# Kernel optimization log

Hardware: AMD Instinct MI355X
Metric: run time of the kernel (lower is better)

Reference implementation:

```python
import jax, jax.numpy as jnp
import numpy as np

T, B, D, H = 1024, 64, 1024, 30  # seq_len, batch, input_size, hidden_size


def setup_inputs() -> dict:
    key = jax.random.key(0)
    ks = jax.random.split(key, 11)
    sc = 1.0 / np.sqrt(H)  # torch default init scale ~ U(-1/sqrt(H), 1/sqrt(H))
    u = lambda k, shape: jax.random.uniform(k, shape, dtype=jnp.float32, minval=-sc, maxval=sc)
    return {
        "x": jax.random.normal(ks[0], (T, B, D), dtype=jnp.float32),
        "W_ih0": u(ks[1], (4 * H, D)),
        "W_hh0": u(ks[2], (4 * H, H)),
        "b_ih0": u(ks[3], (4 * H,)),
        "b_hh0": u(ks[4], (4 * H,)),
        "W_ih1": u(ks[5], (4 * H, H)),
        "W_hh1": u(ks[6], (4 * H, H)),
        "b_ih1": u(ks[7], (4 * H,)),
        "b_hh1": u(ks[8], (4 * H,)),
        "W_out": u(ks[9], (1, H)),
        "b_out": u(ks[10], (1,)),
    }


def _lstm_layer(xs, Wih, Whh, bih, bhh):
    # xs: [T, B, Din] -> hs: [T, B, H]. PyTorch gate order: i, f, g, o.
    xg = jnp.einsum("tbd,gd->tbg", xs, Wih) + (bih + bhh)  # precompute input projection
    h0 = jnp.zeros((xs.shape[1], H), xs.dtype)
    c0 = jnp.zeros((xs.shape[1], H), xs.dtype)

    def step(carry, xw):
        h, c = carry
        gates = xw + h @ Whh.T  # [B, 4H]
        i, f, g, o = jnp.split(gates, 4, axis=-1)
        c = jax.nn.sigmoid(f) * c + jax.nn.sigmoid(i) * jnp.tanh(g)
        h = jax.nn.sigmoid(o) * jnp.tanh(c)
        return (h, c), h

    _, hs = jax.lax.scan(step, (h0, c0), xg)
    return hs


def reference(x, W_ih0, W_hh0, b_ih0, b_hh0, W_ih1, W_hh1, b_ih1, b_hh1, W_out, b_out):
    h1 = _lstm_layer(x, W_ih0, W_hh0, b_ih0, b_hh0)   # layer 0
    h2 = _lstm_layer(h1, W_ih1, W_hh1, b_ih1, b_hh1)  # layer 1
    return h2 @ W_out.T + b_out  # [T, B, 1]
```

## Files before the change

### kernel.cpp

```cpp
#include <hip/hip_runtime.h>
#include <hip/hip_bf16.h>
#include <cstdint>

#define TT 1024
#define BB 64
#define DD 1024
#define HH 30
#define G4 120

typedef __attribute__((ext_vector_type(8))) short short8;
typedef __attribute__((ext_vector_type(4))) float float4v;

__device__ __forceinline__ float frcp(float x) { return __builtin_amdgcn_rcpf(x); }
__device__ __forceinline__ float fsig(float x) { return frcp(1.0f + __expf(-x)); }
__device__ __forceinline__ float ftan(float x) {
    return 2.0f * frcp(1.0f + __expf(-2.0f * x)) - 1.0f;
}
__device__ __forceinline__ float bcast(float v, int l) {
    return __int_as_float(__builtin_amdgcn_readlane(__float_as_int(v), l));
}
__device__ __forceinline__ unsigned short bf16_rne(float f) {
    unsigned u = __float_as_uint(f);
    return (unsigned short)((u + 0x7FFFu + ((u >> 16) & 1u)) >> 16);
}

__global__ void prep_kernel(const float* __restrict__ Wih0,
                            const float* __restrict__ bih0,
                            const float* __restrict__ bhh0,
                            unsigned short* __restrict__ Bhi,
                            unsigned short* __restrict__ Blo,
                            float* __restrict__ bias0) {
    int idx = blockIdx.x * 256 + threadIdx.x;
    int l  = idx & 63;
    int kc = (idx >> 6) & 31;
    int nt = idx >> 11;
    int n = nt * 16 + (l & 15);
    int kb = kc * 32 + (l >> 4) * 8;
    size_t o = (size_t)idx * 8;
#pragma unroll
    for (int j = 0; j < 8; ++j) {
        float wv = (n < G4) ? Wih0[(size_t)n * DD + kb + j] : 0.0f;
        unsigned short hi = bf16_rne(wv);
        float fhi = __uint_as_float((unsigned)hi << 16);
        unsigned short lo = bf16_rne(wv - fhi);
        Bhi[o + j] = hi;
        Blo[o + j] = lo;
    }
    if (idx < 128) bias0[idx] = (idx < G4) ? (bih0[idx] + bhh0[idx]) : 0.0f;
}

__global__ __launch_bounds__(256) void gemm_xg(
    const float* __restrict__ x, const unsigned short* __restrict__ Bhi,
    const unsigned short* __restrict__ Blo, const float* __restrict__ bias0,
    float* __restrict__ xgp) {
    const int tid = threadIdx.x;
    const int w = tid >> 6;
    const int l = tid & 63;
    const int lm = l & 15, lq = l >> 4;
    const int r0 = blockIdx.x * 128 + w * 32;

    float4v acc[2][8];
#pragma unroll
    for (int mt = 0; mt < 2; ++mt)
#pragma unroll
        for (int nt = 0; nt < 8; ++nt) acc[mt][nt] = (float4v)0.0f;

    const float* aptr[2];
    aptr[0] = x + (size_t)(r0 + lm) * DD + lq * 8;
    aptr[1] = x + (size_t)(r0 + 16 + lm) * DD + lq * 8;

    float4 pa[2][2];
#pragma unroll
    for (int mt = 0; mt < 2; ++mt) {
        pa[mt][0] = *(const float4*)(aptr[mt]);
        pa[mt][1] = *(const float4*)(aptr[mt] + 4);
    }

    for (int kc = 0; kc < 32; ++kc) {
        short8 ahi[2], alo[2];
#pragma unroll
        for (int mt = 0; mt < 2; ++mt) {
            float f[8] = {pa[mt][0].x, pa[mt][0].y, pa[mt][0].z, pa[mt][0].w,
                          pa[mt][1].x, pa[mt][1].y, pa[mt][1].z, pa[mt][1].w};
#pragma unroll
            for (int i = 0; i < 8; ++i) {
                unsigned ub = __float_as_uint(f[i]);
                ahi[mt][i] = (short)(ub >> 16);
                float fr = f[i] - __uint_as_float(ub & 0xFFFF0000u);
                alo[mt][i] = (short)(__float_as_uint(fr) >> 16);
            }
        }
        if (kc + 1 < 32) {
            const int ko = (kc + 1) * 32;
#pragma unroll
            for (int mt = 0; mt < 2; ++mt) {
                pa[mt][0] = *(const float4*)(aptr[mt] + ko);
                pa[mt][1] = *(const float4*)(aptr[mt] + ko + 4);
            }
        }
#pragma unroll
        for (int nt = 0; nt < 8; ++nt) {
            const size_t bo = ((size_t)(nt * 32 + kc) * 64 + l) * 8;
            short8 bh = *(const short8*)(Bhi + bo);
            short8 bl = *(const short8*)(Blo + bo);
            acc[0][nt] = __builtin_amdgcn_mfma_f32_16x16x32_bf16(ahi[0], bh, acc[0][nt], 0, 0, 0);
            acc[1][nt] = __builtin_amdgcn_mfma_f32_16x16x32_bf16(ahi[1], bh, acc[1][nt], 0, 0, 0);
            acc[0][nt] = __builtin_amdgcn_mfma_f32_16x16x32_bf16(alo[0], bh, acc[0][nt], 0, 0, 0);
            acc[1][nt] = __builtin_amdgcn_mfma_f32_16x16x32_bf16(alo[1], bh, acc[1][nt], 0, 0, 0);
            acc[0][nt] = __builtin_amdgcn_mfma_f32_16x16x32_bf16(ahi[0], bl, acc[0][nt], 0, 0, 0);
            acc[1][nt] = __builtin_amdgcn_mfma_f32_16x16x32_bf16(ahi[1], bl, acc[1][nt], 0, 0, 0);
        }
    }

#pragma unroll
    for (int nt = 0; nt < 8; ++nt) {
        const int g = nt * 16 + lm;
        if (g < G4) {
            const int gm = g % 60;
            const int lane_t = (gm < HH) ? gm : (32 + gm - HH);
            const int slot = g / 60;
            const float bb = bias0[g];
#pragma unroll
            for (int mt = 0; mt < 2; ++mt)
#pragma unroll
                for (int i = 0; i < 4; ++i) {
                    const size_t row = r0 + mt * 16 + lq * 4 + i;
                    xgp[(row * 64 + lane_t) * 2 + slot] = acc[mt][nt][i] + bb;
                }
        }
    }
}

__global__ __launch_bounds__(128, 1) void lstm_rec(
    const float* __restrict__ xgp, const float* __restrict__ Whh0,
    const float* __restrict__ Wih1, const float* __restrict__ Whh1,
    const float* __restrict__ bih1, const float* __restrict__ bhh1,
    float* __restrict__ h2buf) {
    const int tid = threadIdx.x;
    const int wv = tid >> 6;
    const int l = tid & 63;
    const int b = blockIdx.x;
    const int u = l & 31;
    const int half = l >> 5;
    const bool al = (u < HH);
    const int rlo = half * HH + (al ? u : 0);
    const int rhi = 60 + rlo;

    __shared__ float2 pg[2][64];

    float wa[HH], wb[HH], wc[HH], wd[HH];
    float b1lo = 0.f, b1hi = 0.f;
    if (wv == 0) {
#pragma unroll
        for (int j = 0; j < HH; ++j) {
            wa[j] = al ? Whh0[rlo * HH + j] : 0.f;
            wb[j] = al ? Whh0[rhi * HH + j] : 0.f;
            wc[j] = al ? Wih1[rlo * HH + j] : 0.f;
            wd[j] = al ? Wih1[rhi * HH + j] : 0.f;
        }
        b1lo = al ? (bih1[rlo] + bhh1[rlo]) : 0.f;
        b1hi = al ? (bih1[rhi] + bhh1[rhi]) : 0.f;
    } else {
#pragma unroll
        for (int j = 0; j < HH; ++j) {
            wa[j] = al ? Whh1[rlo * HH + j] : 0.f;
            wb[j] = al ? Whh1[rhi * HH + j] : 0.f;
            wc[j] = 0.f; wd[j] = 0.f;
        }
    }

    float hstate = 0.f, cstate = 0.f;
    float hb[HH];
#pragma unroll
    for (int j = 0; j < HH; ++j) hb[j] = 0.f;

    const float2* xgptr = (const float2*)xgp + (size_t)b * 64 + l;
    float2 xq[4];
    if (wv == 0) {
#pragma unroll
        for (int p = 0; p < 4; ++p) xq[p] = xgptr[(size_t)p * (BB * 64)];
    }

    for (int t = 0; t <= TT; ++t) {
        if (wv == 0) {
            if (t < TT) {
                float2 xw = xq[t & 3];
                const int tn = (t + 4 < TT) ? t + 4 : TT - 1;
                xq[t & 3] = xgptr[(size_t)tn * (BB * 64)];

                float aA = xw.x, aB = 0.f, cA = xw.y, cB = 0.f;
#pragma unroll
                for (int j = 0; j < HH; j += 2) {
                    aA = fmaf(wa[j], hb[j], aA);
                    cA = fmaf(wb[j], hb[j], cA);
                    aB = fmaf(wa[j + 1], hb[j + 1], aB);
                    cB = fmaf(wb[j + 1], hb[j + 1], cB);
                }
                float alo = aA + aB, ahi = cA + cB;
                float plo = __shfl_xor(alo, 32, 64);
                float phi = __shfl_xor(ahi, 32, 64);
                float ipre = half ? plo : alo;
                float fpre = half ? alo : plo;
                float gpre = half ? phi : ahi;
                float opre = half ? ahi : phi;
                cstate = fsig(fpre) * cstate + fsig(ipre) * ftan(gpre);
                hstate = fsig(opre) * ftan(cstate);
#pragma unroll
                for (int j = 0; j < HH; ++j) hb[j] = bcast(hstate, j);

                float zA = b1lo, zB = 0.f, yA = b1hi, yB = 0.f;
#pragma unroll
                for (int j = 0; j < HH; j += 2) {
                    zA = fmaf(wc[j], hb[j], zA);
                    yA = fmaf(wd[j], hb[j], yA);
                    zB = fmaf(wc[j + 1], hb[j + 1], zB);
                    yB = fmaf(wd[j + 1], hb[j + 1], yB);
                }
                pg[t & 1][l] = make_float2(zA + zB, yA + yB);
            }
        } else {
            if (t > 0) {
                const int s = t - 1;
                float2 part = pg[s & 1][l];
                float zA = part.x, zB = 0.f, yA = part.y, yB = 0.f;
#pragma unroll
                for (int j = 0; j < HH; j += 2) {
                    zA = fmaf(wa[j], hb[j], zA);
                    yA = fmaf(wb[j], hb[j], yA);
                    zB = fmaf(wa[j + 1], hb[j + 1], zB);
                    yB = fmaf(wb[j + 1], hb[j + 1], yB);
                }
                float zlo = zA + zB, zhi = yA + yB;
                float qlo = __shfl_xor(zlo, 32, 64);
                float qhi = __shfl_xor(zhi, 32, 64);
                float ipre = half ? qlo : zlo;
                float fpre = half ? zlo : qlo;
                float gpre = half ? qhi : zhi;
                float opre = half ? zhi : qhi;
                cstate = fsig(fpre) * cstate + fsig(ipre) * ftan(gpre);
                hstate = fsig(opre) * ftan(cstate);
#pragma unroll
                for (int j = 0; j < HH; ++j) hb[j] = bcast(hstate, j);
                if (l < HH) h2buf[((size_t)s * BB + b) * 32 + l] = hstate;
            }
        }
        __syncthreads();
    }
}

__global__ __launch_bounds__(256) void out_proj(
    const float* __restrict__ h2buf, const float* __restrict__ Wout,
    const float* __restrict__ bout, float* __restrict__ out) {
    __shared__ float wos[32];
    if (threadIdx.x < 32)
        wos[threadIdx.x] = (threadIdx.x < HH) ? Wout[threadIdx.x] : 0.0f;
    __syncthreads();
    const int idx = blockIdx.x * 256 + threadIdx.x;
    const float4* hp = (const float4*)(h2buf + (size_t)idx * 32);
    float s0 = 0.f, s1 = 0.f;
#pragma unroll
    for (int q = 0; q < 8; ++q) {
        float4 h = hp[q];
        s0 = fmaf(h.x, wos[q * 4 + 0], s0);
        s1 = fmaf(h.y, wos[q * 4 + 1], s1);
        s0 = fmaf(h.z, wos[q * 4 + 2], s0);
        s1 = fmaf(h.w, wos[q * 4 + 3], s1);
    }
    out[idx] = s0 + s1 + bout[0];
}

extern "C" void kernel_launch(void* const* d_in, const int* in_sizes, int n_in,
                              void* d_out, int out_size, void* d_ws, size_t ws_size,
                              hipStream_t stream) {
    const float* x    = (const float*)d_in[0];
    const float* Wih0 = (const float*)d_in[1];
    const float* Whh0 = (const float*)d_in[2];
    const float* bih0 = (const float*)d_in[3];
    const float* bhh0 = (const float*)d_in[4];
    const float* Wih1 = (const float*)d_in[5];
    const float* Whh1 = (const float*)d_in[6];
    const float* bih1 = (const float*)d_in[7];
    const float* bhh1 = (const float*)d_in[8];
    const float* Wout = (const float*)d_in[9];
    const float* bout = (const float*)d_in[10];
    float* out = (float*)d_out;

    char* ws = (char*)d_ws;
    unsigned short* Bhi = (unsigned short*)ws;
    unsigned short* Blo = (unsigned short*)(ws + 262144);
    float* bias0 = (float*)(ws + 524288);
    float* xgp   = (float*)(ws + 1024 * 1024);
    float* h2buf = (float*)(ws + 36 * 1024 * 1024);

    prep_kernel<<<64, 256, 0, stream>>>(Wih0, bih0, bhh0, Bhi, Blo, bias0);
    gemm_xg<<<512, 256, 0, stream>>>(x, Bhi, Blo, bias0, xgp);
    lstm_rec<<<BB, 128, 0, stream>>>(xgp, Whh0, Wih1, Whh1, bih1, bhh1, h2buf);
    out_proj<<<256, 256, 0, stream>>>(h2buf, Wout, bout, out);
}
```

Before: 1.066 ms.

## Fuse input-projection GEMM with LSTM recurrence via producer/consumer flag pipeline

Merges the xg GEMM and the recurrent LSTM kernel into one launch: 64 producer blocks compute GEMM tiles in time order and bump per-group atomic counters, while 64 consumer blocks spin on those counters before prefetching each time chunk. This lets the serial recurrence start as soon as the first time steps are projected, overlapping GEMM work with recurrence instead of running them back to back. The costs are fewer GEMM blocks (64 blocks doing 8 rounds each), spin-wait polling, consumer blocks now launched with 256 threads where two waves sit idle, and reliance on all 128 blocks being co-resident to avoid deadlock.

```diff
diff --git a/kernel.cpp b/kernel.cpp
--- a/kernel.cpp
+++ b/kernel.cpp
@@ -8,6 +8,11 @@
 #define HH 30
 #define G4 120
 
+#define NPROD 64
+#define NROUND 8
+#define GBLK 16
+#define NGRP 32
+
 typedef __attribute__((ext_vector_type(8))) short short8;
 typedef __attribute__((ext_vector_type(4))) float float4v;
 
@@ -29,7 +34,8 @@
                             const float* __restrict__ bhh0,
                             unsigned short* __restrict__ Bhi,
                             unsigned short* __restrict__ Blo,
-                            float* __restrict__ bias0) {
+                            float* __restrict__ bias0,
+                            unsigned* __restrict__ cnt) {
     int idx = blockIdx.x * 256 + threadIdx.x;
     int l  = idx & 63;
     int kc = (idx >> 6) & 31;
@@ -47,106 +53,118 @@
         Blo[o + j] = lo;
     }
     if (idx < 128) bias0[idx] = (idx < G4) ? (bih0[idx] + bhh0[idx]) : 0.0f;
-}
-
-__global__ __launch_bounds__(256) void gemm_xg(
+    if (idx < NGRP) cnt[idx] = 0u;
+}
+
+__global__ __launch_bounds__(256, 2) void fused_fwd(
     const float* __restrict__ x, const unsigned short* __restrict__ Bhi,
     const unsigned short* __restrict__ Blo, const float* __restrict__ bias0,
-    float* __restrict__ xgp) {
-    const int tid = threadIdx.x;
-    const int w = tid >> 6;
-    const int l = tid & 63;
-    const int lm = l & 15, lq = l >> 4;
-    const int r0 = blockIdx.x * 128 + w * 32;
-
-    float4v acc[2][8];
-#pragma unroll
-    for (int mt = 0; mt < 2; ++mt)
-#pragma unroll
-        for (int nt = 0; nt < 8; ++nt) acc[mt][nt] = (float4v)0.0f;
-
-    const float* aptr[2];
-    aptr[0] = x + (size_t)(r0 + lm) * DD + lq * 8;
-    aptr[1] = x + (size_t)(r0 + 16 + lm) * DD + lq * 8;
-
-    float4 pa[2][2];
-#pragma unroll
-    for (int mt = 0; mt < 2; ++mt) {
-        pa[mt][0] = *(const float4*)(aptr[mt]);
-        pa[mt][1] = *(const float4*)(aptr[mt] + 4);
-    }
-
-    for (int kc = 0; kc < 32; ++kc) {
-        short8 ahi[2], alo[2];
-#pragma unroll
-        for (int mt = 0; mt < 2; ++mt) {
-            float f[8] = {pa[mt][0].x, pa[mt][0].y, pa[mt][0].z, pa[mt][0].w,
-                          pa[mt][1].x, pa[mt][1].y, pa[mt][1].z, pa[mt][1].w};
-#pragma unroll
-            for (int i = 0; i < 8; ++i) {
-                unsigned ub = __float_as_uint(f[i]);
-                ahi[mt][i] = (short)(ub >> 16);
-                float fr = f[i] - __uint_as_float(ub & 0xFFFF0000u);
-                alo[mt][i] = (short)(__float_as_uint(fr) >> 16);
-            }
-        }
-        if (kc + 1 < 32) {
-            const int ko = (kc + 1) * 32;
-#pragma unroll
-            for (int mt = 0; mt < 2; ++mt) {
-                pa[mt][0] = *(const float4*)(aptr[mt] + ko);
-                pa[mt][1] = *(const float4*)(aptr[mt] + ko + 4);
-            }
-        }
-#pragma unroll
-        for (int nt = 0; nt < 8; ++nt) {
-            const size_t bo = ((size_t)(nt * 32 + kc) * 64 + l) * 8;
-            short8 bh = *(const short8*)(Bhi + bo);
-            short8 bl = *(const short8*)(Blo + bo);
-            acc[0][nt] = __builtin_amdgcn_mfma_f32_16x16x32_bf16(ahi[0], bh, acc[0][nt], 0, 0, 0);
-            acc[1][nt] = __builtin_amdgcn_mfma_f32_16x16x32_bf16(ahi[1], bh, acc[1][nt], 0, 0, 0);
-            acc[0][nt] = __builtin_amdgcn_mfma_f32_16x16x32_bf16(alo[0], bh, acc[0][nt], 0, 0, 0);
-            acc[1][nt] = __builtin_amdgcn_mfma_f32_16x16x32_bf16(alo[1], bh, acc[1][nt], 0, 0, 0);
-            acc[0][nt] = __builtin_amdgcn_mfma_f32_16x16x32_bf16(ahi[0], bl, acc[0][nt], 0, 0, 0);
-            acc[1][nt] = __builtin_amdgcn_mfma_f32_16x16x32_bf16(ahi[1], bl, acc[1][nt], 0, 0, 0);
-        }
-    }
-
-#pragma unroll
-    for (int nt = 0; nt < 8; ++nt) {
-        const int g = nt * 16 + lm;
-        if (g < G4) {
-            const int gm = g % 60;
-            const int lane_t = (gm < HH) ? gm : (32 + gm - HH);
-            const int slot = g / 60;
-            const float bb = bias0[g];
-#pragma unroll
-            for (int mt = 0; mt < 2; ++mt)
-#pragma unroll
-                for (int i = 0; i < 4; ++i) {
-                    const size_t row = r0 + mt * 16 + lq * 4 + i;
-                    xgp[(row * 64 + lane_t) * 2 + slot] = acc[mt][nt][i] + bb;
-                }
-        }
-    }
-}
-
-__global__ __launch_bounds__(128, 1) void lstm_rec(
-    const float* __restrict__ xgp, const float* __restrict__ Whh0,
+    float* __restrict__ xgp, const float* __restrict__ Whh0,
     const float* __restrict__ Wih1, const float* __restrict__ Whh1,
     const float* __restrict__ bih1, const float* __restrict__ bhh1,
-    float* __restrict__ h2buf) {
+    float* __restrict__ h2buf, unsigned* __restrict__ cnt) {
+
+    __shared__ float2 pg[2][64];
     const int tid = threadIdx.x;
+
+    if (blockIdx.x < NPROD) {
+        const int pb = blockIdx.x;
+        const int w = tid >> 6;
+        const int l = tid & 63;
+        const int lm = l & 15, lq = l >> 4;
+
+        for (int r = 0; r < NROUND; ++r) {
+            const int tile = r * NPROD + pb;
+            const int r0 = tile * 128 + w * 32;
+
+            float4v acc[2][8];
+#pragma unroll
+            for (int mt = 0; mt < 2; ++mt)
+#pragma unroll
+                for (int nt = 0; nt < 8; ++nt) acc[mt][nt] = (float4v)0.0f;
+
+            const float* aptr[2];
+            aptr[0] = x + (size_t)(r0 + lm) * DD + lq * 8;
+            aptr[1] = x + (size_t)(r0 + 16 + lm) * DD + lq * 8;
+
+            float4 pa[2][2];
+#pragma unroll
+            for (int mt = 0; mt < 2; ++mt) {
+                pa[mt][0] = *(const float4*)(aptr[mt]);
+                pa[mt][1] = *(const float4*)(aptr[mt] + 4);
+            }
+
+            for (int kc = 0; kc < 32; ++kc) {
+                short8 ahi[2], alo[2];
+#pragma unroll
+                for (int mt = 0; mt < 2; ++mt) {
+                    float f[8] = {pa[mt][0].x, pa[mt][0].y, pa[mt][0].z, pa[mt][0].w,
+                                  pa[mt][1].x, pa[mt][1].y, pa[mt][1].z, pa[mt][1].w};
+#pragma unroll
+                    for (int i = 0; i < 8; ++i) {
+                        unsigned ub = __float_as_uint(f[i]);
+                        ahi[mt][i] = (short)(ub >> 16);
+                        float fr = f[i] - __uint_as_float(ub & 0xFFFF0000u);
+                        alo[mt][i] = (short)(__float_as_uint(fr) >> 16);
+                    }
+                }
+                if (kc + 1 < 32) {
+                    const int ko = (kc + 1) * 32;
+#pragma unroll
+                    for (int mt = 0; mt < 2; ++mt) {
+                        pa[mt][0] = *(const float4*)(aptr[mt] + ko);
+                        pa[mt][1] = *(const float4*)(aptr[mt] + ko + 4);
+                    }
+                }
+#pragma unroll
+                for (int nt = 0; nt < 8; ++nt) {
+                    const size_t bo = ((size_t)(nt * 32 + kc) * 64 + l) * 8;
+                    short8 bh = *(const short8*)(Bhi + bo);
+                    short8 bl = *(const short8*)(Blo + bo);
+                    acc[0][nt] = __builtin_amdgcn_mfma_f32_16x16x32_bf16(ahi[0], bh, acc[0][nt], 0, 0, 0);
+                    acc[1][nt] = __builtin_amdgcn_mfma_f32_16x16x32_bf16(ahi[1], bh, acc[1][nt], 0, 0, 0);
+                    acc[0][nt] = __builtin_amdgcn_mfma_f32_16x16x32_bf16(alo[0], bh, acc[0][nt], 0, 0, 0);
+                    acc[1][nt] = __builtin_amdgcn_mfma_f32_16x16x32_bf16(alo[1], bh, acc[1][nt], 0, 0, 0);
+                    acc[0][nt] = __builtin_amdgcn_mfma_f32_16x16x32_bf16(ahi[0], bl, acc[0][nt], 0, 0, 0);
+                    acc[1][nt] = __builtin_amdgcn_mfma_f32_16x16x32_bf16(ahi[1], bl, acc[1][nt], 0, 0, 0);
+                }
+            }
+
+#pragma unroll
+            for (int nt = 0; nt < 8; ++nt) {
+                const int g = nt * 16 + lm;
+                if (g < G4) {
+                    const int gm = g % 60;
+                    const int lane_t = (gm < HH) ? gm : (32 + gm - HH);
+                    const int slot = g / 60;
+                    const float bb = bias0[g];
+#pragma unroll
+                    for (int mt = 0; mt < 2; ++mt)
+#pragma unroll
+                        for (int i = 0; i < 4; ++i) {
+                            const size_t row = r0 + mt * 16 + lq * 4 + i;
+                            xgp[(row * 64 + lane_t) * 2 + slot] = acc[mt][nt][i] + bb;
+                        }
+                }
+            }
+            __syncthreads();
+            if (tid == 0) {
+                __threadfence();
+                __hip_atomic_fetch_add(&cnt[tile >> 4], 1u, __ATOMIC_RELEASE,
+                                       __HIP_MEMORY_SCOPE_AGENT);
+            }
+        }
+        return;
+    }
+
     const int wv = tid >> 6;
     const int l = tid & 63;
-    const int b = blockIdx.x;
+    const int b = blockIdx.x - NPROD;
     const int u = l & 31;
     const int half = l >> 5;
     const bool al = (u < HH);
     const int rlo = half * HH + (al ? u : 0);
     const int rhi = 60 + rlo;
-
-    __shared__ float2 pg[2][64];
 
     float wa[HH], wb[HH], wc[HH], wd[HH];
     float b1lo = 0.f, b1hi = 0.f;
@@ -160,7 +178,7 @@
         }
         b1lo = al ? (bih1[rlo] + bhh1[rlo]) : 0.f;
         b1hi = al ? (bih1[rhi] + bhh1[rhi]) : 0.f;
-    } else {
+    } else if (wv == 1) {
 #pragma unroll
         for (int j = 0; j < HH; ++j) {
             wa[j] = al ? Whh1[rlo * HH + j] : 0.f;
@@ -176,7 +194,11 @@
 
     const float2* xgptr = (const float2*)xgp + (size_t)b * 64 + l;
     float2 xq[4];
+    unsigned next_g = 0;
     if (wv == 0) {
+        while (__hip_atomic_load(&cnt[0], __ATOMIC_ACQUIRE, __HIP_MEMORY_SCOPE_AGENT) < GBLK)
+            __builtin_amdgcn_s_sleep(8);
+        next_g = 1;
 #pragma unroll
         for (int p = 0; p < 4; ++p) xq[p] = xgptr[(size_t)p * (BB * 64)];
     }
@@ -186,6 +208,13 @@
             if (t < TT) {
                 float2 xw = xq[t & 3];
                 const int tn = (t + 4 < TT) ? t + 4 : TT - 1;
+                const unsigned gneed = (unsigned)(tn >> 5);
+                if (gneed >= next_g) {
+                    while (__hip_atomic_load(&cnt[gneed], __ATOMIC_ACQUIRE,
+                                             __HIP_MEMORY_SCOPE_AGENT) < GBLK)
+                        __builtin_amdgcn_s_sleep(8);
+                    next_g = gneed + 1;
+                }
                 xq[t & 3] = xgptr[(size_t)tn * (BB * 64)];
 
                 float aA = xw.x, aB = 0.f, cA = xw.y, cB = 0.f;
@@ -218,7 +247,7 @@
                 }
                 pg[t & 1][l] = make_float2(zA + zB, yA + yB);
             }
-        } else {
+        } else if (wv == 1) {
             if (t > 0) {
                 const int s = t - 1;
                 float2 part = pg[s & 1][l];
@@ -289,11 +318,13 @@
     unsigned short* Bhi = (unsigned short*)ws;
     unsigned short* Blo = (unsigned short*)(ws + 262144);
     float* bias0 = (float*)(ws + 524288);
+    unsigned* cnt = (unsigned*)(ws + 524800);
     float* xgp   = (float*)(ws + 1024 * 1024);
     float* h2buf = (float*)(ws + 36 * 1024 * 1024);
 
-    prep_kernel<<<64, 256, 0, stream>>>(Wih0, bih0, bhh0, Bhi, Blo, bias0);
-    gemm_xg<<<512, 256, 0, stream>>>(x, Bhi, Blo, bias0, xgp);
-    lstm_rec<<<BB, 128, 0, stream>>>(xgp, Whh0, Wih1, Whh1, bih1, bhh1, h2buf);
+    prep_kernel<<<64, 256, 0, stream>>>(Wih0, bih0, bhh0, Bhi, Blo, bias0, cnt);
+    fused_fwd<<<NPROD + BB, 256, 0, stream>>>(x, Bhi, Blo, bias0, xgp,
+                                              Whh0, Wih1, Whh1, bih1, bhh1,
+                                              h2buf, cnt);
     out_proj<<<256, 256, 0, stream>>>(h2buf, Wout, bout, out);
 }
```

New measurement: 1.053 ms. No clear change (-1.2%).
